# Kernel optimization log

Measured on AMD Instinct MI355X. Metric: run time of the kernel, lower is better.

The kernel has to match this reference:

```python
import jax, jax.numpy as jnp
import numpy as np

N = 300000; E = N - 1; A = 150000; D = 64; H = 128; T = 512
NEG_SLOPE = 0.2


def _gatv2(h, src, dst, Wl, bl, Wr, br, att, bias):
    # PyG GATv2Conv, heads=1, add_self_loops=False
    xl = h @ Wl + bl            # source transform [N,H]
    xr = h @ Wr + br            # target transform [N,H]
    e = xl[src] + xr[dst]       # [E,H]
    a = jax.nn.leaky_relu(e, NEG_SLOPE) @ att   # [E]
    amax = jax.ops.segment_max(a, dst, num_segments=N)
    ex = jnp.exp(a - amax[dst])
    denom = jax.ops.segment_sum(ex, dst, num_segments=N)
    alpha = ex / (denom[dst] + 1e-16)
    out = jax.ops.segment_sum(alpha[:, None] * xl[src], dst, num_segments=N)
    return out + bias


def setup_inputs() -> dict:
    ks = jax.random.split(jax.random.key(0), 32)
    s = 0.02
    inp = {
        'x': jax.random.normal(ks[0], (N, D), jnp.float32),
        'edge_index': jax.random.randint(ks[1], (2, E), 0, N),
        'focal_seq': jax.random.normal(ks[2], (1, D), jnp.float32),
        'child_idx': jax.random.randint(ks[3], (A,), 0, N),
        'parent_idx': jax.random.randint(ks[4], (A,), 0, N + 1) - 1,  # include -1 (no parent)
        'time_idx': jax.random.randint(ks[5], (A,), 0, T),
        'W_embed': jax.random.normal(ks[6], (D, H)) * s, 'b_embed': jnp.zeros((H,)),
        'bu_Wl': jax.random.normal(ks[7], (H, H)) * s, 'bu_bl': jnp.zeros((H,)),
        'bu_Wr': jax.random.normal(ks[8], (H, H)) * s, 'bu_br': jnp.zeros((H,)),
        'bu_att': jax.random.normal(ks[9], (H,)) * s, 'bu_bias': jnp.zeros((H,)),
        'td_Wl': jax.random.normal(ks[10], (H, H)) * s, 'td_bl': jnp.zeros((H,)),
        'td_Wr': jax.random.normal(ks[11], (H, H)) * s, 'td_br': jnp.zeros((H,)),
        'td_att': jax.random.normal(ks[12], (H,)) * s, 'td_bias': jnp.zeros((H,)),
        'time_table': jax.random.normal(ks[13], (T, H)) * s,
        'W_comb': jax.random.normal(ks[14], (2 * H, H)) * s, 'b_comb': jnp.zeros((H,)),
        'W_a1': jax.random.normal(ks[15], (3 * H, H)) * s, 'b_a1': jnp.zeros((H,)),
        'W_a2': jax.random.normal(ks[16], (H, 1)) * s, 'b_a2': jnp.zeros((1,)),
        'W_seq': jax.random.normal(ks[17], (D, H)) * s, 'b_seq': jnp.zeros((H,)),
    }
    return inp


def reference(x, edge_index, focal_seq, child_idx, parent_idx, time_idx,
              W_embed, b_embed,
              bu_Wl, bu_bl, bu_Wr, bu_br, bu_att, bu_bias,
              td_Wl, td_bl, td_Wr, td_br, td_att, td_bias,
              time_table, W_comb, b_comb, W_a1, b_a1, W_a2, b_a2,
              W_seq, b_seq):
    h = x @ W_embed + b_embed                       # [N,H]
    # bottom-up pass: edge_index flipped -> src=row1, dst=row0
    h_bu = _gatv2(h, edge_index[1], edge_index[0], bu_Wl, bu_bl, bu_Wr, bu_br, bu_att, bu_bias)
    h = h + jax.nn.relu(h_bu)
    # top-down pass: src=row0, dst=row1
    h_td = _gatv2(h, edge_index[0], edge_index[1], td_Wl, td_bl, td_Wr, td_br, td_att, td_bias)
    h = h + jax.nn.relu(h_td)
    context = focal_seq @ W_seq + b_seq             # [1,H]
    h_child = h[child_idx]                          # [A,H]
    h_parent = jnp.where((parent_idx == -1)[:, None], 0.0, h[parent_idx])
    branch = jnp.concatenate([h_child, h_parent], axis=-1) @ W_comb + b_comb  # [A,H]
    t_emb = time_table[time_idx]                    # [A,H]
    combined = jnp.concatenate([branch, t_emb, jnp.broadcast_to(context, (branch.shape[0], context.shape[1]))], axis=-1)  # [A,3H]
    logits = jax.nn.relu(combined @ W_a1 + b_a1) @ W_a2 + b_a2  # [A,1]
    return logits
```

## Files before the change

### kernel.cpp

```cpp
#include <hip/hip_runtime.h>
#include <hip/hip_bf16.h>

#define NN 300000
#define EE 299999
#define AA 150000
#define DD 64
#define HH 128
#define TT 512
#define SCAN_NB ((NN + 1023) / 1024)

typedef unsigned short u16;
typedef unsigned int u32;
typedef __attribute__((ext_vector_type(8))) short short8;
typedef __attribute__((ext_vector_type(4))) float f32x4;

__device__ __forceinline__ float bfb(u16 u) { return __uint_as_float(((u32)u) << 16); }
__device__ __forceinline__ u16 f2b(float f) {
    u32 u = __float_as_uint(f);
    u32 r = (u + 0x7FFFu + ((u >> 16) & 1u)) >> 16;
    return (u16)r;
}
__device__ __forceinline__ uint4 load8(const u16* p) { return *(const uint4*)p; }
__device__ __forceinline__ uint4 load8(const float* p) {
    float4 f1 = *(const float4*)p;
    float4 f2 = *(const float4*)(p + 4);
    union { ushort s[8]; uint4 v; } u;
    u.s[0] = f2b(f1.x); u.s[1] = f2b(f1.y); u.s[2] = f2b(f1.z); u.s[3] = f2b(f1.w);
    u.s[4] = f2b(f2.x); u.s[5] = f2b(f2.y); u.s[6] = f2b(f2.z); u.s[7] = f2b(f2.w);
    return u.v;
}
__device__ __forceinline__ void unpack8(uint4 v, float* f) {
    u32 w0 = v.x, w1 = v.y, w2 = v.z, w3 = v.w;
    f[0] = bfb((u16)w0); f[1] = bfb((u16)(w0 >> 16));
    f[2] = bfb((u16)w1); f[3] = bfb((u16)(w1 >> 16));
    f[4] = bfb((u16)w2); f[5] = bfb((u16)(w2 >> 16));
    f[6] = bfb((u16)w3); f[7] = bfb((u16)(w3 >> 16));
}
__device__ __forceinline__ int swo(int row, int kblock) {
    return row * 64 + ((kblock ^ (row & 7)) * 8);
}
__device__ __forceinline__ void gl_lds16(const u16* src, u16* ldsbase) {
    __builtin_amdgcn_global_load_lds((const __attribute__((address_space(1))) u32*)src,
                                     (__attribute__((address_space(3))) u32*)ldsbase, 16, 0, 0);
}

__global__ __launch_bounds__(256) void k_wtrans(const float* w0, const float* w1,
                                                const float* w2, const float* w3,
                                                const float* w4, const float* w5,
                                                const float* w6, const float* w7,
                                                u16* __restrict__ wt) {
    int widx = blockIdx.x >> 3, part = blockIdx.x & 7;
    const float* W; int K = 128;
    switch (widx) {
        case 0: W = w0; break; case 1: W = w1; break;
        case 2: W = w2; break; case 3: W = w3; break;
        case 4: W = w4; break; case 5: W = w5; break;
        case 6: W = w6; break; default: W = w7; K = 64; break;
    }
    u16* dst = wt + widx * 16384;
    int total = K * 128;
    int lo = part * 2048, hi = lo + 2048;
    if (hi > total) hi = total;
    for (int idx = lo + threadIdx.x; idx < hi; idx += 256) {
        int k = idx >> 7, n = idx & 127;
        dst[n * K + k] = f2b(W[k * 128 + n]);
    }
}

__global__ void k_ctx_c1(const float* __restrict__ focal, const float* __restrict__ Wseq,
                         const float* __restrict__ bseq, const float* __restrict__ Wa1c,
                         const float* __restrict__ ba1, float* __restrict__ c1) {
    __shared__ float cs[HH];
    int t = threadIdx.x;
    float acc = bseq[t];
    for (int d = 0; d < DD; ++d) acc = fmaf(focal[d], Wseq[d * HH + t], acc);
    cs[t] = acc;
    __syncthreads();
    float a2 = ba1[t];
    for (int k = 0; k < HH; ++k) a2 = fmaf(cs[k], Wa1c[k * HH + t], a2);
    c1[t] = a2;
}

__global__ void k_tproj(const float* __restrict__ tt, const float* __restrict__ Wa1m,
                        float* __restrict__ tproj) {
    int ti = blockIdx.x, t = threadIdx.x;
    float acc = 0.f;
    for (int k = 0; k < HH; ++k)
        acc = fmaf(tt[ti * HH + k], Wa1m[k * HH + t], acc);
    tproj[(size_t)ti * HH + t] = acc;
}

__global__ void k_hist(const int* __restrict__ dst, int* __restrict__ counts) {
    int e = blockIdx.x * 256 + threadIdx.x;
    if (e < EE) atomicAdd(&counts[dst[e]], 1);
}

__global__ __launch_bounds__(256) void k_scan_block(const int* __restrict__ in,
                                                    int* __restrict__ out,
                                                    int* __restrict__ bsum, int n) {
    __shared__ int sh[256];
    int b = blockIdx.x, t = threadIdx.x;
    int base = b * 1024 + t * 4;
    int v0 = (base + 0 < n) ? in[base + 0] : 0;
    int v1 = (base + 1 < n) ? in[base + 1] : 0;
    int v2 = (base + 2 < n) ? in[base + 2] : 0;
    int v3 = (base + 3 < n) ? in[base + 3] : 0;
    int tsum = v0 + v1 + v2 + v3;
    sh[t] = tsum;
    __syncthreads();
    for (int d = 1; d < 256; d <<= 1) {
        int x = (t >= d) ? sh[t - d] : 0;
        __syncthreads();
        sh[t] += x;
        __syncthreads();
    }
    int excl = sh[t] - tsum;
    if (t == 255) bsum[b] = sh[255];
    if (base + 0 < n) out[base + 0] = excl;
    if (base + 1 < n) out[base + 1] = excl + v0;
    if (base + 2 < n) out[base + 2] = excl + v0 + v1;
    if (base + 3 < n) out[base + 3] = excl + v0 + v1 + v2;
}

__global__ __launch_bounds__(256) void k_scan_top(int* __restrict__ data, int n) {
    __shared__ int sh[256];
    int t = threadIdx.x;
    int base = t * 4;
    int v0 = (base + 0 < n) ? data[base + 0] : 0;
    int v1 = (base + 1 < n) ? data[base + 1] : 0;
    int v2 = (base + 2 < n) ? data[base + 2] : 0;
    int v3 = (base + 3 < n) ? data[base + 3] : 0;
    int tsum = v0 + v1 + v2 + v3;
    sh[t] = tsum;
    __syncthreads();
    for (int d = 1; d < 256; d <<= 1) {
        int x = (t >= d) ? sh[t - d] : 0;
        __syncthreads();
        sh[t] += x;
        __syncthreads();
    }
    int excl = sh[t] - tsum;
    if (base + 0 < n) data[base + 0] = excl;
    if (base + 1 < n) data[base + 1] = excl + v0;
    if (base + 2 < n) data[base + 2] = excl + v0 + v1;
    if (base + 3 < n) data[base + 3] = excl + v0 + v1 + v2;
}

__global__ void k_scan_add(int* __restrict__ out, const int* __restrict__ bsum, int n) {
    int i = blockIdx.x * 256 + threadIdx.x;
    if (i < n) out[i] += bsum[i >> 10];
}

__global__ void k_settail(int* o1, int* o2) {
    if (threadIdx.x == 0) { o1[NN] = EE; o2[NN] = EE; }
}

__global__ void k_scatter(const int* __restrict__ src, const int* __restrict__ dst,
                          int* __restrict__ cursor, int* __restrict__ elist) {
    int e = blockIdx.x * 256 + threadIdx.x;
    if (e >= EE) return;
    int pos = atomicAdd(&cursor[dst[e]], 1);
    elist[pos] = src[e];
}

template <int K, typename InT>
__global__ __launch_bounds__(256) void k_mfma_proj(const InT* __restrict__ in,
                                                   const u16* __restrict__ WT,
                                                   const float* __restrict__ bias,
                                                   u16* __restrict__ out, int nrows) {
    __shared__ u16 lds[17408];
    u16* a_lds = lds;
    u16* b_lds = lds + 8192;
    u16* clds = lds;
    const int t = threadIdx.x;
    const int tile_m = blockIdx.x * 128;
    const int wave = t >> 6, l = t & 15, quad = (t >> 4) & 3;
    const int wr = wave >> 1, wc = wave & 1;
    f32x4 acc[4][4] = {};

    for (int chunk = 0; chunk < K / 64; ++chunk) {
        const int c0 = chunk * 64;
        __syncthreads();
        for (int ci = t; ci < 1024; ci += 256) {
            int row = ci >> 3, kc = ci & 7;
            int grow = tile_m + row;
            uint4 v = make_uint4(0, 0, 0, 0);
            if (grow < nrows) v = load8(&in[(size_t)grow * K + c0 + kc * 8]);
            *(uint4*)&a_lds[swo(row, kc)] = v;
        }
        for (int ci = t; ci < 1024; ci += 256) {
            int n = ci >> 3, kc = ci & 7;
            *(uint4*)&b_lds[swo(n, kc)] = *(const uint4*)&WT[(size_t)n * K + c0 + kc * 8];
        }
        __syncthreads();
#pragma unroll
        for (int ks = 0; ks < 2; ++ks) {
            short8 af[4], bf[4];
#pragma unroll
            for (int i = 0; i < 4; ++i)
                af[i] = *(const short8*)&a_lds[swo(wr * 64 + i * 16 + l, ks * 4 + quad)];
#pragma unroll
            for (int j = 0; j < 4; ++j)
                bf[j] = *(const short8*)&b_lds[swo(wc * 64 + j * 16 + l, ks * 4 + quad)];
#pragma unroll
            for (int i = 0; i < 4; ++i)
#pragma unroll
                for (int j = 0; j < 4; ++j)
                    acc[i][j] = __builtin_amdgcn_mfma_f32_16x16x32_bf16(af[i], bf[j], acc[i][j], 0, 0, 0);
        }
    }
    __syncthreads();
#pragma unroll
    for (int j = 0; j < 4; ++j) {
        int col = wc * 64 + j * 16 + l;
        float b = bias[col];
#pragma unroll
        for (int i = 0; i < 4; ++i) {
            int rloc = wr * 64 + i * 16 + quad * 4;
#pragma unroll
            for (int r = 0; r < 4; ++r)
                clds[(rloc + r) * 136 + col] = f2b(acc[i][j][r] + b);
        }
    }
    __syncthreads();
#pragma unroll
    for (int it = 0; it < 8; ++it) {
        int idx = it * 256 + t;
        int row = idx >> 4, c16 = idx & 15;
        int grow = tile_m + row;
        if (grow < nrows)
            *(uint4*)&out[(size_t)grow * HH + c16 * 8] = *(const uint4*)&clds[row * 136 + c16 * 8];
    }
}

__global__ __launch_bounds__(256) void k_mfma_proj2(const u16* __restrict__ in,
                                                    const u16* __restrict__ WT1,
                                                    const u16* __restrict__ WT2,
                                                    const float* __restrict__ b1,
                                                    const float* __restrict__ b2,
                                                    u16* __restrict__ out1,
                                                    u16* __restrict__ out2, int nrows) {
    __shared__ u16 lds[24576];
    u16* a_lds = lds;
    u16* b1_lds = lds + 8192;
    u16* b2_lds = lds + 16384;
    u16* clds = lds;
    const int t = threadIdx.x;
    const int tile_m = blockIdx.x * 128;
    const int wave = t >> 6, l = t & 15, quad = (t >> 4) & 3;
    const int wr = wave >> 1, wc = wave & 1;
    f32x4 acc1[4][4] = {}, acc2[4][4] = {};

    for (int chunk = 0; chunk < 2; ++chunk) {
        const int c0 = chunk * 64;
        __syncthreads();
#pragma unroll
        for (int it = 0; it < 4; ++it) {
            int ci = it * 256 + t;
            int row = ci >> 3;
            int colblk = ((ci & 7) ^ (row & 7)) * 8;
            u16* wbase = lds + (ci & ~63) * 8;
            int grow = tile_m + row; if (grow >= nrows) grow = nrows - 1;
            gl_lds16(&in[(size_t)grow * HH + c0 + colblk], wbase);
            gl_lds16(&WT1[(size_t)row * HH + c0 + colblk], wbase + 8192);
            gl_lds16(&WT2[(size_t)row * HH + c0 + colblk], wbase + 16384);
        }
        __syncthreads();
#pragma unroll
        for (int ks = 0; ks < 2; ++ks) {
            short8 af[4], bf1[4], bf2[4];
#pragma unroll
            for (int i = 0; i < 4; ++i)
                af[i] = *(const short8*)&a_lds[swo(wr * 64 + i * 16 + l, ks * 4 + quad)];
#pragma unroll
            for (int j = 0; j < 4; ++j) {
                bf1[j] = *(const short8*)&b1_lds[swo(wc * 64 + j * 16 + l, ks * 4 + quad)];
                bf2[j] = *(const short8*)&b2_lds[swo(wc * 64 + j * 16 + l, ks * 4 + quad)];
            }
#pragma unroll
            for (int i = 0; i < 4; ++i)
#pragma unroll
                for (int j = 0; j < 4; ++j) {
                    acc1[i][j] = __builtin_amdgcn_mfma_f32_16x16x32_bf16(af[i], bf1[j], acc1[i][j], 0, 0, 0);
                    acc2[i][j] = __builtin_amdgcn_mfma_f32_16x16x32_bf16(af[i], bf2[j], acc2[i][j], 0, 0, 0);
                }
        }
    }
    __syncthreads();
#pragma unroll
    for (int j = 0; j < 4; ++j) {
        int col = wc * 64 + j * 16 + l;
        float b = b1[col];
#pragma unroll
        for (int i = 0; i < 4; ++i) {
            int rloc = wr * 64 + i * 16 + quad * 4;
#pragma unroll
            for (int r = 0; r < 4; ++r)
                clds[(rloc + r) * 136 + col] = f2b(acc1[i][j][r] + b);
        }
    }
    __syncthreads();
#pragma unroll
    for (int it = 0; it < 8; ++it) {
        int idx = it * 256 + t;
        int row = idx >> 4, c16 = idx & 15;
        int grow = tile_m + row;
        if (grow < nrows)
            *(uint4*)&out1[(size_t)grow * HH + c16 * 8] = *(const uint4*)&clds[row * 136 + c16 * 8];
    }
    __syncthreads();
#pragma unroll
    for (int j = 0; j < 4; ++j) {
        int col = wc * 64 + j * 16 + l;
        float b = b2[col];
#pragma unroll
        for (int i = 0; i < 4; ++i) {
            int rloc = wr * 64 + i * 16 + quad * 4;
#pragma unroll
            for (int r = 0; r < 4; ++r)
                clds[(rloc + r) * 136 + col] = f2b(acc2[i][j][r] + b);
        }
    }
    __syncthreads();
#pragma unroll
    for (int it = 0; it < 8; ++it) {
        int idx = it * 256 + t;
        int row = idx >> 4, c16 = idx & 15;
        int grow = tile_m + row;
        if (grow < nrows)
            *(uint4*)&out2[(size_t)grow * HH + c16 * 8] = *(const uint4*)&clds[row * 136 + c16 * 8];
    }
}

__global__ __launch_bounds__(256) void k_mfma_gproj(const u16* __restrict__ h,
                                                    const int* __restrict__ idx1,
                                                    const int* __restrict__ idx2,
                                                    const u16* __restrict__ WT1,
                                                    const u16* __restrict__ WT2,
                                                    const float* __restrict__ bias,
                                                    u16* __restrict__ out, int nrows) {
    __shared__ u16 lds[17408];
    u16* a_lds = lds;
    u16* b_lds = lds + 8192;
    u16* clds = lds;
    const int t = threadIdx.x;
    const int tile_m = blockIdx.x * 128;
    const int wave = t >> 6, l = t & 15, quad = (t >> 4) & 3;
    const int wr = wave >> 1, wc = wave & 1;
    f32x4 acc[4][4] = {};

    for (int pass = 0; pass < 2; ++pass) {
        const int* idx = pass ? idx2 : idx1;
        const u16* WT = pass ? WT2 : WT1;
        for (int chunk = 0; chunk < 2; ++chunk) {
            const int c0 = chunk * 64;
            __syncthreads();
            int gneg[4];
#pragma unroll
            for (int it = 0; it < 4; ++it) {
                int ci = it * 256 + t;
                int row = ci >> 3;
                int colblk = ((ci & 7) ^ (row & 7)) * 8;
                u16* wbase = lds + (ci & ~63) * 8;
                int item = tile_m + row; if (item >= nrows) item = nrows - 1;
                int g = idx[item];
                gneg[it] = (g < 0);
                if (g < 0) g = 0;
                gl_lds16(&h[(size_t)g * HH + c0 + colblk], wbase);
                gl_lds16(&WT[(size_t)row * HH + c0 + colblk], wbase + 8192);
            }
            __syncthreads();
#pragma unroll
            for (int it = 0; it < 4; ++it) {
                if (gneg[it]) {
                    int ci = it * 256 + t;
                    *(uint4*)&a_lds[ci * 8] = make_uint4(0, 0, 0, 0);
                }
            }
            __syncthreads();
#pragma unroll
            for (int ks = 0; ks < 2; ++ks) {
                short8 af[4], bf[4];
#pragma unroll
                for (int i = 0; i < 4; ++i)
                    af[i] = *(const short8*)&a_lds[swo(wr * 64 + i * 16 + l, ks * 4 + quad)];
#pragma unroll
                for (int j = 0; j < 4; ++j)
                    bf[j] = *(const short8*)&b_lds[swo(wc * 64 + j * 16 + l, ks * 4 + quad)];
#pragma unroll
                for (int i = 0; i < 4; ++i)
#pragma unroll
                    for (int j = 0; j < 4; ++j)
                        acc[i][j] = __builtin_amdgcn_mfma_f32_16x16x32_bf16(af[i], bf[j], acc[i][j], 0, 0, 0);
            }
        }
    }
    __syncthreads();
#pragma unroll
    for (int j = 0; j < 4; ++j) {
        int col = wc * 64 + j * 16 + l;
        float b = bias[col];
#pragma unroll
        for (int i = 0; i < 4; ++i) {
            int rloc = wr * 64 + i * 16 + quad * 4;
#pragma unroll
            for (int r = 0; r < 4; ++r)
                clds[(rloc + r) * 136 + col] = f2b(acc[i][j][r] + b);
        }
    }
    __syncthreads();
#pragma unroll
    for (int it = 0; it < 8; ++it) {
        int idx = it * 256 + t;
        int row = idx >> 4, c16 = idx & 15;
        int item = tile_m + row;
        if (item < nrows)
            *(uint4*)&out[(size_t)item * HH + c16 * 8] = *(const uint4*)&clds[row * 136 + c16 * 8];
    }
}

__global__ __launch_bounds__(256) void k_mfma_zlogit(const u16* __restrict__ branch,
                                                     const int* __restrict__ time_idx,
                                                     const float* __restrict__ tproj,
                                                     const float* __restrict__ c1,
                                                     const u16* __restrict__ WTa1,
                                                     const float* __restrict__ Wa2,
                                                     const float* __restrict__ ba2,
                                                     float* __restrict__ out) {
    __shared__ u16 lds[16384];
    u16* a_lds = lds;
    u16* b_lds = lds + 8192;
    __shared__ float red[2][128];
    const int t = threadIdx.x;
    const int tile_m = blockIdx.x * 128;
    const int wave = t >> 6, l = t & 15, quad = (t >> 4) & 3;
    const int wr = wave >> 1, wc = wave & 1;
    f32x4 acc[4][4] = {};

    for (int chunk = 0; chunk < 2; ++chunk) {
        const int c0 = chunk * 64;
        __syncthreads();
#pragma unroll
        for (int it = 0; it < 4; ++it) {
            int ci = it * 256 + t;
            int row = ci >> 3;
            int colblk = ((ci & 7) ^ (row & 7)) * 8;
            u16* wbase = lds + (ci & ~63) * 8;
            int item = tile_m + row; if (item >= AA) item = AA - 1;
            gl_lds16(&branch[(size_t)item * HH + c0 + colblk], wbase);
            gl_lds16(&WTa1[(size_t)row * HH + c0 + colblk], wbase + 8192);
        }
        __syncthreads();
#pragma unroll
        for (int ks = 0; ks < 2; ++ks) {
            short8 af[4], bf[4];
#pragma unroll
            for (int i = 0; i < 4; ++i)
                af[i] = *(const short8*)&a_lds[swo(wr * 64 + i * 16 + l, ks * 4 + quad)];
#pragma unroll
            for (int j = 0; j < 4; ++j)
                bf[j] = *(const short8*)&b_lds[swo(wc * 64 + j * 16 + l, ks * 4 + quad)];
#pragma unroll
            for (int i = 0; i < 4; ++i)
#pragma unroll
                for (int j = 0; j < 4; ++j)
                    acc[i][j] = __builtin_amdgcn_mfma_f32_16x16x32_bf16(af[i], bf[j], acc[i][j], 0, 0, 0);
        }
    }
    float c1v[4], wa2v[4];
#pragma unroll
    for (int j = 0; j < 4; ++j) {
        int col = wc * 64 + j * 16 + l;
        c1v[j] = c1[col];
        wa2v[j] = Wa2[col];
    }
#pragma unroll
    for (int i = 0; i < 4; ++i) {
        int rbase = tile_m + wr * 64 + i * 16 + quad * 4;
#pragma unroll
        for (int r = 0; r < 4; ++r) {
            int item = rbase + r;
            int ti = (item < AA) ? time_idx[item] : 0;
            const float* tp = tproj + (size_t)ti * HH;
            float partial = 0.f;
#pragma unroll
            for (int j = 0; j < 4; ++j) {
                int col = wc * 64 + j * 16 + l;
                float z = fmaxf(acc[i][j][r] + tp[col] + c1v[j], 0.f);
                partial = fmaf(z, wa2v[j], partial);
            }
            partial += __shfl_xor(partial, 1);
            partial += __shfl_xor(partial, 2);
            partial += __shfl_xor(partial, 4);
            partial += __shfl_xor(partial, 8);
            if (l == 0) red[wc][wr * 64 + i * 16 + quad * 4 + r] = partial;
        }
    }
    __syncthreads();
    if (t < 128) {
        int item = tile_m + t;
        if (item < AA) out[item] = red[0][t] + red[1][t] + ba2[0];
    }
}

__global__ __launch_bounds__(256) void k_gat_fused(u16* __restrict__ h,
                                                   const u16* __restrict__ xl,
                                                   const u16* __restrict__ xr,
                                                   const int* __restrict__ offs,
                                                   const int* __restrict__ elist,
                                                   const float* __restrict__ att,
                                                   const float* __restrict__ bias) {
    int g = blockIdx.x * 16 + (threadIdx.x >> 4);
    int l = threadIdx.x & 15;
    float attv[8], biasv[8];
    *(float4*)&attv[0] = *(const float4*)&att[l * 8];
    *(float4*)&attv[4] = *(const float4*)&att[l * 8 + 4];
    *(float4*)&biasv[0] = *(const float4*)&bias[l * 8];
    *(float4*)&biasv[4] = *(const float4*)&bias[l * 8 + 4];
    float xrf[8];
    unpack8(*(const uint4*)&xr[(size_t)g * HH + l * 8], xrf);
    int e0 = offs[g], e1 = offs[g + 1];

    float m = -__builtin_inff(), s = 0.f;
    float acc[8] = {};
    for (int e = e0; e < e1; ++e) {
        int sidx = elist[e];
        float xf[8];
        unpack8(*(const uint4*)&xl[(size_t)sidx * HH + l * 8], xf);
        float p = 0.f;
#pragma unroll
        for (int j = 0; j < 8; ++j) {
            float v = xf[j] + xrf[j];
            v = v >= 0.f ? v : 0.2f * v;
            p = fmaf(v, attv[j], p);
        }
        p += __shfl_xor(p, 1); p += __shfl_xor(p, 2);
        p += __shfl_xor(p, 4); p += __shfl_xor(p, 8);
        float mn = fmaxf(m, p);
        float so = __expf(m - mn);
        float w = __expf(p - mn);
        s = s * so + w;
#pragma unroll
        for (int j = 0; j < 8; ++j) acc[j] = fmaf(acc[j], so, w * xf[j]);
        m = mn;
    }
    float inv = 1.f / (s + 1e-16f);

    float hf[8];
    unpack8(*(const uint4*)&h[(size_t)g * HH + l * 8], hf);
    union { ushort sh[8]; uint4 v; } o;
#pragma unroll
    for (int j = 0; j < 8; ++j) {
        hf[j] += fmaxf(fmaf(acc[j], inv, biasv[j]), 0.f);
        o.sh[j] = f2b(hf[j]);
    }
    *(uint4*)&h[(size_t)g * HH + l * 8] = o.v;
}

typedef const float* fp;

static void build_csr(const int* src, const int* dst, int* offs, int* elist,
                      int* work, int* bsum, hipStream_t stream) {
    hipMemsetAsync(work, 0, (size_t)NN * 4, stream);
    k_hist<<<(EE + 255) / 256, 256, 0, stream>>>(dst, work);
    k_scan_block<<<SCAN_NB, 256, 0, stream>>>(work, offs, bsum, NN);
    k_scan_top<<<1, 256, 0, stream>>>(bsum, SCAN_NB);
    k_scan_add<<<(NN + 255) / 256, 256, 0, stream>>>(offs, bsum, NN);
    hipMemcpyAsync(work, offs, (size_t)NN * 4, hipMemcpyDeviceToDevice, stream);
    k_scatter<<<(EE + 255) / 256, 256, 0, stream>>>(src, dst, work, elist);
}

extern "C" void kernel_launch(void* const* d_in, const int* in_sizes, int n_in,
                              void* d_out, int out_size, void* d_ws, size_t ws_size,
                              hipStream_t stream) {
    fp x                 = (fp)d_in[0];
    const int* ei        = (const int*)d_in[1];
    fp focal             = (fp)d_in[2];
    const int* child_idx = (const int*)d_in[3];
    const int* parent_idx= (const int*)d_in[4];
    const int* time_idx  = (const int*)d_in[5];
    fp W_embed = (fp)d_in[6],  b_embed = (fp)d_in[7];
    fp bu_Wl   = (fp)d_in[8],  bu_bl   = (fp)d_in[9];
    fp bu_Wr   = (fp)d_in[10], bu_br   = (fp)d_in[11];
    fp bu_att  = (fp)d_in[12], bu_bias = (fp)d_in[13];
    fp td_Wl   = (fp)d_in[14], td_bl   = (fp)d_in[15];
    fp td_Wr   = (fp)d_in[16], td_br   = (fp)d_in[17];
    fp td_att  = (fp)d_in[18], td_bias = (fp)d_in[19];
    fp time_table = (fp)d_in[20];
    fp W_comb  = (fp)d_in[21], b_comb  = (fp)d_in[22];
    fp W_a1    = (fp)d_in[23], b_a1    = (fp)d_in[24];
    fp W_a2    = (fp)d_in[25], b_a2    = (fp)d_in[26];
    fp W_seq   = (fp)d_in[27], b_seq   = (fp)d_in[28];

    const size_t NH = (size_t)NN * HH;
    u16* wt = (u16*)d_ws;
    u16* h  = wt + 8 * 16384;
    u16* xl = h + NH;
    u16* xr = xl + NH;
    u16* branch = xl;
    float* c1v   = (float*)(xr + NH);
    float* tproj = c1v + HH;
    int* offsBU  = (int*)(tproj + (size_t)TT * HH);
    int* offsTD  = offsBU + NN + 1;
    int* elistBU = offsTD + NN + 1;
    int* elistTD = elistBU + EE;
    int* csr_work= elistTD + EE;
    int* bsum    = csr_work + NN;

    build_csr(ei + EE, ei, offsBU, elistBU, csr_work, bsum, stream);
    build_csr(ei, ei + EE, offsTD, elistTD, csr_work, bsum, stream);
    k_settail<<<1, 64, 0, stream>>>(offsBU, offsTD);

    k_wtrans<<<64, 256, 0, stream>>>(bu_Wl, bu_Wr, td_Wl, td_Wr,
                                     W_comb, W_comb + (size_t)HH * HH, W_a1, W_embed, wt);
    const u16* wt_buWl = wt + 0 * 16384;
    const u16* wt_buWr = wt + 1 * 16384;
    const u16* wt_tdWl = wt + 2 * 16384;
    const u16* wt_tdWr = wt + 3 * 16384;
    const u16* wt_combC = wt + 4 * 16384;
    const u16* wt_combP = wt + 5 * 16384;
    const u16* wt_a1   = wt + 6 * 16384;
    const u16* wt_embed = wt + 7 * 16384;

    k_ctx_c1<<<1, 128, 0, stream>>>(focal, W_seq, b_seq, W_a1 + (size_t)256 * HH, b_a1, c1v);
    k_tproj<<<TT, 128, 0, stream>>>(time_table, W_a1 + (size_t)128 * HH, tproj);

    const int NB = (NN + 127) / 128;
    k_mfma_proj<64, float><<<NB, 256, 0, stream>>>(x, wt_embed, b_embed, h, NN);

    k_mfma_proj2<<<NB, 256, 0, stream>>>(h, wt_buWl, wt_buWr, bu_bl, bu_br, xl, xr, NN);
    k_gat_fused<<<NN / 16, 256, 0, stream>>>(h, xl, xr, offsBU, elistBU, bu_att, bu_bias);

    k_mfma_proj2<<<NB, 256, 0, stream>>>(h, wt_tdWl, wt_tdWr, td_bl, td_br, xl, xr, NN);
    k_gat_fused<<<NN / 16, 256, 0, stream>>>(h, xl, xr, offsTD, elistTD, td_att, td_bias);

    k_mfma_gproj<<<(AA + 127) / 128, 256, 0, stream>>>(
        h, child_idx, parent_idx, wt_combC, wt_combP, b_comb, branch, AA);

    k_mfma_zlogit<<<(AA + 127) / 128, 256, 0, stream>>>(
        branch, time_idx, tproj, c1v, wt_a1, W_a2, b_a2, (float*)d_out);
}
```

Measured before the change: 570.4 us.

## Fuse branch projection with logit MLP and widen proj2 blocks to 512 threads

The combine projection (child/parent gather times W_comb) and the logit MLP become one kernel. The branch tile is kept in a swizzled LDS buffer, so the [A,H] intermediate never makes a global write and read round trip. Separately, the dual-output projection kernel now runs 512 threads per block, with each wave owning 32 rows instead of 64. This lowers per-thread accumulator registers and raises wave count per tile, at the cost of reloading the B fragments more often per row. The fused kernel uses more LDS per block, which may reduce occupancy.

```diff
diff --git a/kernel.cpp b/kernel.cpp
--- a/kernel.cpp
+++ b/kernel.cpp
@@ -38,6 +38,9 @@
 }
 __device__ __forceinline__ int swo(int row, int kblock) {
     return row * 64 + ((kblock ^ (row & 7)) * 8);
+}
+__device__ __forceinline__ int swo2(int row, int kblock) {
+    return row * 128 + (((kblock & 8) | ((kblock & 7) ^ (row & 7))) * 8);
 }
 __device__ __forceinline__ void gl_lds16(const u16* src, u16* ldsbase) {
     __builtin_amdgcn_global_load_lds((const __attribute__((address_space(1))) u32*)src,
@@ -233,7 +236,7 @@
     }
 }
 
-__global__ __launch_bounds__(256) void k_mfma_proj2(const u16* __restrict__ in,
+__global__ __launch_bounds__(512) void k_mfma_proj2(const u16* __restrict__ in,
                                                     const u16* __restrict__ WT1,
                                                     const u16* __restrict__ WT2,
                                                     const float* __restrict__ b1,
@@ -249,14 +252,14 @@
     const int tile_m = blockIdx.x * 128;
     const int wave = t >> 6, l = t & 15, quad = (t >> 4) & 3;
     const int wr = wave >> 1, wc = wave & 1;
-    f32x4 acc1[4][4] = {}, acc2[4][4] = {};
+    f32x4 acc1[2][4] = {}, acc2[2][4] = {};
 
     for (int chunk = 0; chunk < 2; ++chunk) {
         const int c0 = chunk * 64;
         __syncthreads();
 #pragma unroll
-        for (int it = 0; it < 4; ++it) {
-            int ci = it * 256 + t;
+        for (int it = 0; it < 2; ++it) {
+            int ci = it * 512 + t;
             int row = ci >> 3;
             int colblk = ((ci & 7) ^ (row & 7)) * 8;
             u16* wbase = lds + (ci & ~63) * 8;
@@ -268,17 +271,17 @@
         __syncthreads();
 #pragma unroll
         for (int ks = 0; ks < 2; ++ks) {
-            short8 af[4], bf1[4], bf2[4];
-#pragma unroll
-            for (int i = 0; i < 4; ++i)
-                af[i] = *(const short8*)&a_lds[swo(wr * 64 + i * 16 + l, ks * 4 + quad)];
+            short8 af[2], bf1[4], bf2[4];
+#pragma unroll
+            for (int i = 0; i < 2; ++i)
+                af[i] = *(const short8*)&a_lds[swo(wr * 32 + i * 16 + l, ks * 4 + quad)];
 #pragma unroll
             for (int j = 0; j < 4; ++j) {
                 bf1[j] = *(const short8*)&b1_lds[swo(wc * 64 + j * 16 + l, ks * 4 + quad)];
                 bf2[j] = *(const short8*)&b2_lds[swo(wc * 64 + j * 16 + l, ks * 4 + quad)];
             }
 #pragma unroll
-            for (int i = 0; i < 4; ++i)
+            for (int i = 0; i < 2; ++i)
 #pragma unroll
                 for (int j = 0; j < 4; ++j) {
                     acc1[i][j] = __builtin_amdgcn_mfma_f32_16x16x32_bf16(af[i], bf1[j], acc1[i][j], 0, 0, 0);
@@ -292,8 +295,8 @@
         int col = wc * 64 + j * 16 + l;
         float b = b1[col];
 #pragma unroll
-        for (int i = 0; i < 4; ++i) {
-            int rloc = wr * 64 + i * 16 + quad * 4;
+        for (int i = 0; i < 2; ++i) {
+            int rloc = wr * 32 + i * 16 + quad * 4;
 #pragma unroll
             for (int r = 0; r < 4; ++r)
                 clds[(rloc + r) * 136 + col] = f2b(acc1[i][j][r] + b);
@@ -301,8 +304,8 @@
     }
     __syncthreads();
 #pragma unroll
-    for (int it = 0; it < 8; ++it) {
-        int idx = it * 256 + t;
+    for (int it = 0; it < 4; ++it) {
+        int idx = it * 512 + t;
         int row = idx >> 4, c16 = idx & 15;
         int grow = tile_m + row;
         if (grow < nrows)
@@ -314,8 +317,8 @@
         int col = wc * 64 + j * 16 + l;
         float b = b2[col];
 #pragma unroll
-        for (int i = 0; i < 4; ++i) {
-            int rloc = wr * 64 + i * 16 + quad * 4;
+        for (int i = 0; i < 2; ++i) {
+            int rloc = wr * 32 + i * 16 + quad * 4;
 #pragma unroll
             for (int r = 0; r < 4; ++r)
                 clds[(rloc + r) * 136 + col] = f2b(acc2[i][j][r] + b);
@@ -323,8 +326,8 @@
     }
     __syncthreads();
 #pragma unroll
-    for (int it = 0; it < 8; ++it) {
-        int idx = it * 256 + t;
+    for (int it = 0; it < 4; ++it) {
+        int idx = it * 512 + t;
         int row = idx >> 4, c16 = idx & 15;
         int grow = tile_m + row;
         if (grow < nrows)
@@ -332,17 +335,25 @@
     }
 }
 
-__global__ __launch_bounds__(256) void k_mfma_gproj(const u16* __restrict__ h,
-                                                    const int* __restrict__ idx1,
-                                                    const int* __restrict__ idx2,
-                                                    const u16* __restrict__ WT1,
-                                                    const u16* __restrict__ WT2,
-                                                    const float* __restrict__ bias,
-                                                    u16* __restrict__ out, int nrows) {
-    __shared__ u16 lds[17408];
+__global__ __launch_bounds__(256) void k_branch_logit(const u16* __restrict__ h,
+                                                      const int* __restrict__ idx1,
+                                                      const int* __restrict__ idx2,
+                                                      const u16* __restrict__ WT1,
+                                                      const u16* __restrict__ WT2,
+                                                      const float* __restrict__ bias,
+                                                      const int* __restrict__ time_idx,
+                                                      const float* __restrict__ tproj,
+                                                      const float* __restrict__ c1,
+                                                      const u16* __restrict__ WTa1,
+                                                      const float* __restrict__ Wa2,
+                                                      const float* __restrict__ ba2,
+                                                      float* __restrict__ out) {
+    __shared__ u16 lds[24576];
+    __shared__ float red[2][128];
     u16* a_lds = lds;
     u16* b_lds = lds + 8192;
-    u16* clds = lds;
+    u16* abuf = lds;
+    u16* z2 = lds + 16384;
     const int t = threadIdx.x;
     const int tile_m = blockIdx.x * 128;
     const int wave = t >> 6, l = t & 15, quad = (t >> 4) & 3;
@@ -362,7 +373,7 @@
                 int row = ci >> 3;
                 int colblk = ((ci & 7) ^ (row & 7)) * 8;
                 u16* wbase = lds + (ci & ~63) * 8;
-                int item = tile_m + row; if (item >= nrows) item = nrows - 1;
+                int item = tile_m + row; if (item >= AA) item = AA - 1;
                 int g = idx[item];
                 gneg[it] = (g < 0);
                 if (g < 0) g = 0;
@@ -400,43 +411,16 @@
     for (int j = 0; j < 4; ++j) {
         int col = wc * 64 + j * 16 + l;
         float b = bias[col];
+        int kb = col >> 3, ko = col & 7;
 #pragma unroll
         for (int i = 0; i < 4; ++i) {
             int rloc = wr * 64 + i * 16 + quad * 4;
 #pragma unroll
             for (int r = 0; r < 4; ++r)
-                clds[(rloc + r) * 136 + col] = f2b(acc[i][j][r] + b);
-        }
-    }
-    __syncthreads();
-#pragma unroll
-    for (int it = 0; it < 8; ++it) {
-        int idx = it * 256 + t;
-        int row = idx >> 4, c16 = idx & 15;
-        int item = tile_m + row;
-        if (item < nrows)
-            *(uint4*)&out[(size_t)item * HH + c16 * 8] = *(const uint4*)&clds[row * 136 + c16 * 8];
-    }
-}
-
-__global__ __launch_bounds__(256) void k_mfma_zlogit(const u16* __restrict__ branch,
-                                                     const int* __restrict__ time_idx,
-                                                     const float* __restrict__ tproj,
-                                                     const float* __restrict__ c1,
-                                                     const u16* __restrict__ WTa1,
-                                                     const float* __restrict__ Wa2,
-                                                     const float* __restrict__ ba2,
-                                                     float* __restrict__ out) {
-    __shared__ u16 lds[16384];
-    u16* a_lds = lds;
-    u16* b_lds = lds + 8192;
-    __shared__ float red[2][128];
-    const int t = threadIdx.x;
-    const int tile_m = blockIdx.x * 128;
-    const int wave = t >> 6, l = t & 15, quad = (t >> 4) & 3;
-    const int wr = wave >> 1, wc = wave & 1;
-    f32x4 acc[4][4] = {};
-
+                abuf[swo2(rloc + r, kb) + ko] = f2b(acc[i][j][r] + b);
+        }
+    }
+    f32x4 accz[4][4] = {};
     for (int chunk = 0; chunk < 2; ++chunk) {
         const int c0 = chunk * 64;
         __syncthreads();
@@ -445,26 +429,25 @@
             int ci = it * 256 + t;
             int row = ci >> 3;
             int colblk = ((ci & 7) ^ (row & 7)) * 8;
-            u16* wbase = lds + (ci & ~63) * 8;
-            int item = tile_m + row; if (item >= AA) item = AA - 1;
-            gl_lds16(&branch[(size_t)item * HH + c0 + colblk], wbase);
-            gl_lds16(&WTa1[(size_t)row * HH + c0 + colblk], wbase + 8192);
+            u16* wbase = z2 + (ci & ~63) * 8;
+            gl_lds16(&WTa1[(size_t)row * HH + c0 + colblk], wbase);
         }
         __syncthreads();
 #pragma unroll
         for (int ks = 0; ks < 2; ++ks) {
             short8 af[4], bf[4];
+            int kb = chunk * 8 + ks * 4 + quad;
 #pragma unroll
             for (int i = 0; i < 4; ++i)
-                af[i] = *(const short8*)&a_lds[swo(wr * 64 + i * 16 + l, ks * 4 + quad)];
+                af[i] = *(const short8*)&abuf[swo2(wr * 64 + i * 16 + l, kb)];
 #pragma unroll
             for (int j = 0; j < 4; ++j)
-                bf[j] = *(const short8*)&b_lds[swo(wc * 64 + j * 16 + l, ks * 4 + quad)];
+                bf[j] = *(const short8*)&z2[swo(wc * 64 + j * 16 + l, ks * 4 + quad)];
 #pragma unroll
             for (int i = 0; i < 4; ++i)
 #pragma unroll
                 for (int j = 0; j < 4; ++j)
-                    acc[i][j] = __builtin_amdgcn_mfma_f32_16x16x32_bf16(af[i], bf[j], acc[i][j], 0, 0, 0);
+                    accz[i][j] = __builtin_amdgcn_mfma_f32_16x16x32_bf16(af[i], bf[j], accz[i][j], 0, 0, 0);
         }
     }
     float c1v[4], wa2v[4];
@@ -486,7 +469,7 @@
 #pragma unroll
             for (int j = 0; j < 4; ++j) {
                 int col = wc * 64 + j * 16 + l;
-                float z = fmaxf(acc[i][j][r] + tp[col] + c1v[j], 0.f);
+                float z = fmaxf(accz[i][j][r] + tp[col] + c1v[j], 0.f);
                 partial = fmaf(z, wa2v[j], partial);
             }
             partial += __shfl_xor(partial, 1);
@@ -597,7 +580,6 @@
     u16* h  = wt + 8 * 16384;
     u16* xl = h + NH;
     u16* xr = xl + NH;
-    u16* branch = xl;
     float* c1v   = (float*)(xr + NH);
     float* tproj = c1v + HH;
     int* offsBU  = (int*)(tproj + (size_t)TT * HH);
@@ -628,15 +610,13 @@
     const int NB = (NN + 127) / 128;
     k_mfma_proj<64, float><<<NB, 256, 0, stream>>>(x, wt_embed, b_embed, h, NN);
 
-    k_mfma_proj2<<<NB, 256, 0, stream>>>(h, wt_buWl, wt_buWr, bu_bl, bu_br, xl, xr, NN);
+    k_mfma_proj2<<<NB, 512, 0, stream>>>(h, wt_buWl, wt_buWr, bu_bl, bu_br, xl, xr, NN);
     k_gat_fused<<<NN / 16, 256, 0, stream>>>(h, xl, xr, offsBU, elistBU, bu_att, bu_bias);
 
-    k_mfma_proj2<<<NB, 256, 0, stream>>>(h, wt_tdWl, wt_tdWr, td_bl, td_br, xl, xr, NN);
+    k_mfma_proj2<<<NB, 512, 0, stream>>>(h, wt_tdWl, wt_tdWr, td_bl, td_br, xl, xr, NN);
     k_gat_fused<<<NN / 16, 256, 0, stream>>>(h, xl, xr, offsTD, elistTD, td_att, td_bias);
 
-    k_mfma_gproj<<<(AA + 127) / 128, 256, 0, stream>>>(
-        h, child_idx, parent_idx, wt_combC, wt_combP, b_comb, branch, AA);
-
-    k_mfma_zlogit<<<(AA + 127) / 128, 256, 0, stream>>>(
-        branch, time_idx, tproj, c1v, wt_a1, W_a2, b_a2, (float*)d_out);
-}
+    k_branch_logit<<<(AA + 127) / 128, 256, 0, stream>>>(
+        h, child_idx, parent_idx, wt_combC, wt_combP, b_comb,
+        time_idx, tproj, c1v, wt_a1, W_a2, b_a2, (float*)d_out);
+}
```

Result: no change. 561.0 us (-1.6%).
